# Kernel tuning notes

Measured on AMD Instinct MI355X. Metric: run time of the kernel, lower is better.

The kernel has to match this reference:

```python
import jax, jax.numpy as jnp
import numpy as np

D_MODEL = 1024
N_HEADS = 16
D_HEAD = D_MODEL // N_HEADS
SCALE = 1.0 / np.sqrt(D_HEAD).astype(np.float32)


def _feature_map(x):
    # phi(x) = elu(x) + 1
    return jax.nn.elu(x) + 1.0


def setup_inputs() -> dict:
    key = jax.random.key(0)
    ks = jax.random.split(key, 7)
    b, s = 4, 2048
    w = 1.0 / np.sqrt(D_MODEL).astype(np.float32)
    return {
        "x": jax.random.normal(ks[0], (b, s, D_MODEL), dtype=jnp.float32),
        "Wq": jax.random.normal(ks[1], (D_MODEL, D_MODEL), dtype=jnp.float32) * w,
        "Wk": jax.random.normal(ks[2], (D_MODEL, D_MODEL), dtype=jnp.float32) * w,
        "Wv": jax.random.normal(ks[3], (D_MODEL, D_MODEL), dtype=jnp.float32) * w,
        "Wo": jax.random.normal(ks[4], (D_MODEL, D_MODEL), dtype=jnp.float32) * w,
        "Wg": jax.random.normal(ks[5], (N_HEADS, D_MODEL), dtype=jnp.float32) * w,
        "bg": jax.random.normal(ks[6], (N_HEADS,), dtype=jnp.float32) * 0.02,
    }


def reference(x, Wq, Wk, Wv, Wo, Wg, bg):
    b, s, _ = x.shape
    # projections (PyTorch Linear: y = x @ W.T)
    q = (x @ Wq.T).reshape(b, s, N_HEADS, D_HEAD)
    k = (x @ Wk.T).reshape(b, s, N_HEADS, D_HEAD)
    v = (x @ Wv.T).reshape(b, s, N_HEADS, D_HEAD)
    q = _feature_map(q * SCALE)
    k = _feature_map(k)
    gate = jax.nn.sigmoid(x @ Wg.T + bg)  # [b, s, h]

    # time-major for scan: [s, b, h, dh] and [s, b, h]
    qt = jnp.moveaxis(q, 1, 0)
    kt = jnp.moveaxis(k, 1, 0)
    vt = jnp.moveaxis(v, 1, 0)
    gt = jnp.moveaxis(gate, 1, 0)

    S0 = jnp.zeros((b, N_HEADS, D_HEAD, D_HEAD), dtype=x.dtype)

    def step(S, inp):
        q_t, k_t, v_t, g_t = inp
        # S_t = g_t * S_{t-1} + k_t v_t^T
        S = g_t[:, :, None, None] * S + k_t[..., :, None] * v_t[..., None, :]
        y_t = jnp.einsum("bhi,bhij->bhj", q_t, S)
        return S, y_t

    _, ys = jax.lax.scan(step, S0, (qt, kt, vt, gt))  # ys: [s, b, h, dh]
    y = jnp.moveaxis(ys, 0, 1).reshape(b, s, D_MODEL)
    return y @ Wo.T
```

## Files before the change

### kernel.cpp

```cpp
#include <hip/hip_runtime.h>
#include <hip/hip_bf16.h>
#include <math.h>

#define BATCH 4
#define SEQ 2048
#define DMODEL 1024
#define NHEADS 16
#define DHEAD 64
#define MTOK (BATCH * SEQ)
#define SCALE_Q 0.125f
#define NCHAIN (BATCH * NHEADS)
#define CT 64
#define NC (SEQ / CT)
#define SP 72
#define QKVS 3072

typedef unsigned short ushort_t;
typedef __attribute__((ext_vector_type(8))) short bf16x8;
typedef __attribute__((ext_vector_type(4))) float f32x4;

__device__ __forceinline__ float bf2f(unsigned short u) {
    return __uint_as_float(((unsigned)u) << 16);
}
__device__ __forceinline__ unsigned short f2bf(float f) {
    unsigned u = __float_as_uint(f);
    return (unsigned short)((u + 0x7fffu + ((u >> 16) & 1u)) >> 16);
}

__global__ __launch_bounds__(256) void cvt_f32_bf16(const float* __restrict__ in,
                                                    ushort_t* __restrict__ out, int n4) {
    int i = blockIdx.x * 256 + threadIdx.x;
    if (i < n4) {
        float4 v = ((const float4*)in)[i];
        ushort4 o;
        o.x = f2bf(v.x); o.y = f2bf(v.y); o.z = f2bf(v.z); o.w = f2bf(v.w);
        ((ushort4*)out)[i] = o;
    }
}

__global__ __launch_bounds__(256) void cvt_weights(const float* __restrict__ Wq,
                                                   const float* __restrict__ Wk,
                                                   const float* __restrict__ Wv,
                                                   const float* __restrict__ Wo,
                                                   ushort_t* __restrict__ dst) {
    int i = blockIdx.x * 256 + threadIdx.x;
    const int row = i >> 8;
    const int c4 = i & 255;
    const float* src;
    if (row < 1024)      src = Wq + (size_t)row * DMODEL;
    else if (row < 2048) src = Wk + (size_t)(row - 1024) * DMODEL;
    else if (row < 3072) src = Wv + (size_t)(row - 2048) * DMODEL;
    else                 src = Wo + (size_t)(row - 3072) * DMODEL;
    float4 v = ((const float4*)src)[c4];
    ushort4 o;
    o.x = f2bf(v.x); o.y = f2bf(v.y); o.z = f2bf(v.z); o.w = f2bf(v.w);
    ((ushort4*)(dst + (size_t)row * DMODEL))[c4] = o;
}

#define GT 128
#define GBK 32

__global__ __launch_bounds__(256) void gemm_bf16(const ushort_t* __restrict__ A,
                                                 const ushort_t* __restrict__ B,
                                                 float* __restrict__ Cf,
                                                 ushort_t* __restrict__ Cb,
                                                 int M, int N, int K,
                                                 int mode) {
    __shared__ ushort_t As[GT * GBK];
    __shared__ ushort_t Bs[GT * GBK];

    const int tid = threadIdx.x;
    const int w = tid >> 6;
    const int l = tid & 63;
    const int m0 = blockIdx.y * GT;
    const int n0 = blockIdx.x * GT;
    const int wm = (w >> 1) * 64;
    const int wn = (w & 1) * 64;

    const int srow = l >> 2;
    const int schunk = (l & 3) * 8;

    f32x4 acc[4][4];
#pragma unroll
    for (int i = 0; i < 4; ++i)
#pragma unroll
        for (int j = 0; j < 4; ++j)
#pragma unroll
            for (int r = 0; r < 4; ++r) acc[i][j][r] = 0.f;

    const int fr = l & 15;
    const int fq = (l >> 4) * 8;

    for (int k0 = 0; k0 < K; k0 += GBK) {
        __syncthreads();
#pragma unroll
        for (int i = 0; i < 2; ++i) {
            const int s = w * 2 + i;
            const ushort_t* ga = A + (size_t)(m0 + s * 16 + srow) * K + k0 + schunk;
            const ushort_t* gb = B + (size_t)(n0 + s * 16 + srow) * K + k0 + schunk;
            __builtin_amdgcn_global_load_lds(
                (const __attribute__((address_space(1))) unsigned int*)(const void*)ga,
                (__attribute__((address_space(3))) unsigned int*)(void*)&As[s * 16 * GBK],
                16, 0, 0);
            __builtin_amdgcn_global_load_lds(
                (const __attribute__((address_space(1))) unsigned int*)(const void*)gb,
                (__attribute__((address_space(3))) unsigned int*)(void*)&Bs[s * 16 * GBK],
                16, 0, 0);
        }
        __syncthreads();

        bf16x8 af[4], bfr[4];
#pragma unroll
        for (int ti = 0; ti < 4; ++ti)
            af[ti] = *(const bf16x8*)&As[(wm + ti * 16 + fr) * GBK + fq];
#pragma unroll
        for (int tj = 0; tj < 4; ++tj)
            bfr[tj] = *(const bf16x8*)&Bs[(wn + tj * 16 + fr) * GBK + fq];
#pragma unroll
        for (int ti = 0; ti < 4; ++ti)
#pragma unroll
            for (int tj = 0; tj < 4; ++tj)
                acc[ti][tj] = __builtin_amdgcn_mfma_f32_16x16x32_bf16(
                    af[ti], bfr[tj], acc[ti][tj], 0, 0, 0);
    }

    float escale = 1.0f;
    bool do_phi = false;
    if (mode == 3) {
        do_phi = (n0 < 2048);
        escale = (n0 < 1024) ? SCALE_Q : 1.0f;
    }

    const int er = (l >> 4) * 4;
    const int ec = l & 15;
#pragma unroll
    for (int ti = 0; ti < 4; ++ti)
#pragma unroll
        for (int tj = 0; tj < 4; ++tj)
#pragma unroll
            for (int r = 0; r < 4; ++r) {
                const int row = m0 + wm + ti * 16 + er + r;
                const int col = n0 + wn + tj * 16 + ec;
                float val = acc[ti][tj][r];
                if (mode == 0) {
                    Cf[(size_t)row * N + col] = val;
                } else {
                    val *= escale;
                    if (do_phi) val = (val > 0.f) ? (val + 1.f) : __expf(val);
                    Cb[(size_t)row * N + col] = f2bf(val);
                }
            }
}

__global__ __launch_bounds__(256) void gate_kernel(const float* __restrict__ x,
                                                   const float* __restrict__ Wg,
                                                   const float* __restrict__ bg,
                                                   float* __restrict__ gate) {
    const int m = blockIdx.x;
    const int tid = threadIdx.x;
    const int h = tid >> 4;
    const int r = tid & 15;

    const float* xr = x + (size_t)m * DMODEL;
    const float* wr = Wg + (size_t)h * DMODEL;

    float p = 0.f;
#pragma unroll
    for (int i = 0; i < 16; ++i) {
        const int k = (r << 2) + (i << 6);
        float4 xv = *(const float4*)&xr[k];
        float4 wv = *(const float4*)&wr[k];
        p += xv.x * wv.x + xv.y * wv.y + xv.z * wv.z + xv.w * wv.w;
    }
    p += __shfl_xor(p, 8, 64);
    p += __shfl_xor(p, 4, 64);
    p += __shfl_xor(p, 2, 64);
    p += __shfl_xor(p, 1, 64);
    if (r == 0) {
        float vv = p + bg[h];
        gate[(size_t)m * NHEADS + h] = 1.f / (1.f + __expf(-vv));
    }
}

__global__ __launch_bounds__(256) void p1_kernel(const ushort_t* __restrict__ qkv,
                                                 const float* __restrict__ gate,
                                                 float* __restrict__ Dt,
                                                 float* __restrict__ Bg) {
    const int tile = blockIdx.x;
    const int chain = tile >> 5;
    const int c = tile & 31;
    const int b = chain >> 4;
    const int h = chain & 15;
    const int tid = threadIdx.x;
    const int w = tid >> 6;
    const int l = tid & 63;

    __shared__ ushort_t Ks[CT * SP];
    __shared__ ushort_t Vs[CT * SP];
    __shared__ float bs[CT];

    {
        const int row = tid >> 2;
        const int seg = (tid & 3) * 16;
        const size_t grow = ((size_t)(b * SEQ + c * CT + row)) * QKVS + h * DHEAD + seg;
        float4 a0 = *(const float4*)&qkv[grow + 1024];
        float4 a1 = *(const float4*)&qkv[grow + 1024 + 8];
        float4 b0 = *(const float4*)&qkv[grow + 2048];
        float4 b1 = *(const float4*)&qkv[grow + 2048 + 8];
        *(float4*)&Ks[row * SP + seg]     = a0;
        *(float4*)&Ks[row * SP + seg + 8] = a1;
        *(float4*)&Vs[row * SP + seg]     = b0;
        *(float4*)&Vs[row * SP + seg + 8] = b1;
    }
    if (tid < 64) {
        float g = gate[((size_t)(b * SEQ + c * CT + tid)) * NHEADS + h];
        float lg = __logf(g);
#pragma unroll
        for (int d = 1; d < 64; d <<= 1) {
            float n = __shfl_up(lg, d, 64);
            if (l >= d) lg += n;
        }
        bs[tid] = lg;
        if (tid == 63) Bg[tile] = lg;
    }
    __syncthreads();

    const float B = bs[63];
    const int fr = l & 15;
    const int fq = (l >> 4) * 8;
    const int jw = w * 16;

    f32x4 accD[4];
#pragma unroll
    for (int nt = 0; nt < 4; ++nt)
#pragma unroll
        for (int r = 0; r < 4; ++r) accD[nt][r] = 0.f;

#pragma unroll
    for (int kc = 0; kc < 2; ++kc) {
        float ef[8];
#pragma unroll
        for (int m = 0; m < 8; ++m) ef[m] = __expf(B - bs[kc * 32 + fq + m]);
        bf16x8 va;
#pragma unroll
        for (int m = 0; m < 8; ++m)
            va[m] = (short)Vs[(kc * 32 + fq + m) * SP + jw + fr];
#pragma unroll
        for (int nt = 0; nt < 4; ++nt) {
            bf16x8 kf;
#pragma unroll
            for (int m = 0; m < 8; ++m)
                kf[m] = (short)f2bf(ef[m] * bf2f(Ks[(kc * 32 + fq + m) * SP + nt * 16 + fr]));
            accD[nt] = __builtin_amdgcn_mfma_f32_16x16x32_bf16(va, kf, accD[nt], 0, 0, 0);
        }
    }

    const int er = (l >> 4) * 4;
    const size_t dbase = (size_t)tile * (DHEAD * DHEAD);
#pragma unroll
    for (int nt = 0; nt < 4; ++nt)
#pragma unroll
        for (int r = 0; r < 4; ++r) {
            const int j = jw + er + r;
            const int i = nt * 16 + fr;
            Dt[dbase + j * DHEAD + i] = accD[nt][r];
        }
}

__global__ __launch_bounds__(256) void p2_kernel(const float* __restrict__ Dt,
                                                 const float* __restrict__ Bg,
                                                 ushort_t* __restrict__ St) {
    const int chain = blockIdx.x >> 2;
    const int jq = (blockIdx.x & 3) * 16;
    const int tid = threadIdx.x;
    const int jj = jq + (tid >> 4);
    const int ii = (tid & 15) * 4;

    float4 S = make_float4(0.f, 0.f, 0.f, 0.f);
    for (int c = 0; c < NC; ++c) {
        const size_t base = (((size_t)chain * NC + c) * DHEAD + jj) * DHEAD + ii;
        ushort4 o;
        o.x = f2bf(S.x); o.y = f2bf(S.y); o.z = f2bf(S.z); o.w = f2bf(S.w);
        *(ushort4*)&St[base] = o;
        const float eB = __expf(Bg[chain * NC + c]);
        const float4 D = *(const float4*)&Dt[base];
        S.x = eB * S.x + D.x;
        S.y = eB * S.y + D.y;
        S.z = eB * S.z + D.z;
        S.w = eB * S.w + D.w;
    }
}

__global__ __launch_bounds__(256) void p3_kernel(const ushort_t* __restrict__ qkv,
                                                 const ushort_t* __restrict__ St,
                                                 const float* __restrict__ gate,
                                                 ushort_t* __restrict__ yb) {
    const int tile = blockIdx.x;
    const int chain = tile >> 5;
    const int c = tile & 31;
    const int b = chain >> 4;
    const int h = chain & 15;
    const int tid = threadIdx.x;
    const int w = tid >> 6;
    const int l = tid & 63;

    __shared__ ushort_t Qs[CT * SP];
    __shared__ ushort_t Ks[CT * SP];
    __shared__ ushort_t Vs[CT * SP];
    __shared__ ushort_t Ss[CT * SP];
    __shared__ ushort_t Ps[CT * SP];
    __shared__ float bs[CT];

    {
        const int row = tid >> 2;
        const int seg = (tid & 3) * 16;
        const size_t grow = ((size_t)(b * SEQ + c * CT + row)) * QKVS + h * DHEAD + seg;
        float4 q0 = *(const float4*)&qkv[grow];
        float4 q1 = *(const float4*)&qkv[grow + 8];
        float4 k0 = *(const float4*)&qkv[grow + 1024];
        float4 k1 = *(const float4*)&qkv[grow + 1024 + 8];
        float4 v0 = *(const float4*)&qkv[grow + 2048];
        float4 v1 = *(const float4*)&qkv[grow + 2048 + 8];
        const size_t srow = (((size_t)chain * NC + c) * DHEAD + row) * DHEAD + seg;
        float4 s0 = *(const float4*)&St[srow];
        float4 s1 = *(const float4*)&St[srow + 8];
        *(float4*)&Qs[row * SP + seg]     = q0;
        *(float4*)&Qs[row * SP + seg + 8] = q1;
        *(float4*)&Ks[row * SP + seg]     = k0;
        *(float4*)&Ks[row * SP + seg + 8] = k1;
        *(float4*)&Vs[row * SP + seg]     = v0;
        *(float4*)&Vs[row * SP + seg + 8] = v1;
        *(float4*)&Ss[row * SP + seg]     = s0;
        *(float4*)&Ss[row * SP + seg + 8] = s1;
    }
    if (tid < 64) {
        float g = gate[((size_t)(b * SEQ + c * CT + tid)) * NHEADS + h];
        float lg = __logf(g);
#pragma unroll
        for (int d = 1; d < 64; d <<= 1) {
            float n = __shfl_up(lg, d, 64);
            if (l >= d) lg += n;
        }
        bs[tid] = lg;
    }
    __syncthreads();

    const int fr = l & 15;
    const int fq = (l >> 4) * 8;
    const int tw = w * 16;

    bf16x8 qa[2];
#pragma unroll
    for (int kc = 0; kc < 2; ++kc)
        qa[kc] = *(const bf16x8*)&Qs[(tw + fr) * SP + kc * 32 + fq];

    f32x4 accA[4], accP[4];
#pragma unroll
    for (int nt = 0; nt < 4; ++nt)
#pragma unroll
        for (int r = 0; r < 4; ++r) { accA[nt][r] = 0.f; accP[nt][r] = 0.f; }

#pragma unroll
    for (int kc = 0; kc < 2; ++kc)
#pragma unroll
        for (int nt = 0; nt < 4; ++nt) {
            bf16x8 sb = *(const bf16x8*)&Ss[(nt * 16 + fr) * SP + kc * 32 + fq];
            accA[nt] = __builtin_amdgcn_mfma_f32_16x16x32_bf16(qa[kc], sb, accA[nt], 0, 0, 0);
            bf16x8 kf = *(const bf16x8*)&Ks[(nt * 16 + fr) * SP + kc * 32 + fq];
            accP[nt] = __builtin_amdgcn_mfma_f32_16x16x32_bf16(qa[kc], kf, accP[nt], 0, 0, 0);
        }

    const int er = (l >> 4) * 4;
    int trow[4];
    float bt[4];
#pragma unroll
    for (int r = 0; r < 4; ++r) { trow[r] = tw + er + r; bt[r] = bs[trow[r]]; }
#pragma unroll
    for (int nt = 0; nt < 4; ++nt) {
        const int tau = nt * 16 + fr;
        const float btau = bs[tau];
#pragma unroll
        for (int r = 0; r < 4; ++r) {
            float f = (tau <= trow[r]) ? __expf(bt[r] - btau) : 0.f;
            Ps[trow[r] * SP + tau] = f2bf(accP[nt][r] * f);
        }
    }
    __syncthreads();

    f32x4 accY[4];
#pragma unroll
    for (int r = 0; r < 4; ++r) {
        const float eb = __expf(bt[r]);
#pragma unroll
        for (int nt = 0; nt < 4; ++nt) accY[nt][r] = accA[nt][r] * eb;
    }
#pragma unroll
    for (int kc = 0; kc < 2; ++kc) {
        bf16x8 pa = *(const bf16x8*)&Ps[(tw + fr) * SP + kc * 32 + fq];
#pragma unroll
        for (int nt = 0; nt < 4; ++nt) {
            bf16x8 vf;
#pragma unroll
            for (int m = 0; m < 8; ++m)
                vf[m] = (short)Vs[(kc * 32 + fq + m) * SP + nt * 16 + fr];
            accY[nt] = __builtin_amdgcn_mfma_f32_16x16x32_bf16(pa, vf, accY[nt], 0, 0, 0);
        }
    }

    const size_t ybase = ((size_t)(b * SEQ + c * CT)) * DMODEL + h * DHEAD;
#pragma unroll
    for (int nt = 0; nt < 4; ++nt)
#pragma unroll
        for (int r = 0; r < 4; ++r)
            yb[ybase + (size_t)trow[r] * DMODEL + nt * 16 + fr] = f2bf(accY[nt][r]);
}

extern "C" void kernel_launch(void* const* d_in, const int* in_sizes, int n_in,
                              void* d_out, int out_size, void* d_ws, size_t ws_size,
                              hipStream_t stream) {
    const float* x  = (const float*)d_in[0];
    const float* Wq = (const float*)d_in[1];
    const float* Wk = (const float*)d_in[2];
    const float* Wv = (const float*)d_in[3];
    const float* Wo = (const float*)d_in[4];
    const float* Wg = (const float*)d_in[5];
    const float* bg = (const float*)d_in[6];
    float* out = (float*)d_out;

    const size_t elems = (size_t)MTOK * DMODEL;
    const size_t welems = (size_t)DMODEL * DMODEL;
    const size_t stelems = (size_t)NCHAIN * NC * DHEAD * DHEAD;

    ushort_t* xb   = (ushort_t*)d_ws;
    ushort_t* qkv  = xb + elems;
    ushort_t* yb   = qkv + (size_t)MTOK * QKVS;
    ushort_t* wcat = yb + elems;
    float* gate    = (float*)(wcat + 4 * welems);
    ushort_t* St   = (ushort_t*)(gate + (size_t)MTOK * NHEADS);
    float* Bg      = (float*)(St + stelems);
    float* Dt      = Bg + (size_t)NCHAIN * NC;

    const size_t need = (size_t)((char*)(Dt + stelems) - (char*)d_ws);
    if (ws_size < need) return;

    cvt_f32_bf16<<<dim3((int)(elems / 4 / 256)), dim3(256), 0, stream>>>(x, xb, (int)(elems / 4));
    cvt_weights<<<dim3((int)(4 * welems / 4 / 256)), dim3(256), 0, stream>>>(Wq, Wk, Wv, Wo, wcat);

    gemm_bf16<<<dim3(QKVS / GT, MTOK / GT), dim3(256), 0, stream>>>(
        xb, wcat, nullptr, qkv, MTOK, QKVS, DMODEL, 3);

    gate_kernel<<<dim3(MTOK), dim3(256), 0, stream>>>(x, Wg, bg, gate);

    p1_kernel<<<dim3(NCHAIN * NC), dim3(256), 0, stream>>>(qkv, gate, Dt, Bg);
    p2_kernel<<<dim3(NCHAIN * 4), dim3(256), 0, stream>>>(Dt, Bg, St);
    p3_kernel<<<dim3(NCHAIN * NC), dim3(256), 0, stream>>>(qkv, St, gate, yb);

    gemm_bf16<<<dim3(DMODEL / GT, MTOK / GT), dim3(256), 0, stream>>>(
        yb, wcat + 3 * welems, out, nullptr, MTOK, DMODEL, DMODEL, 0);
}
```

Baseline: 286.6 us.

## Double-buffer GEMM LDS tiles and XOR-swizzle shared-memory layout

The bf16 MFMA GEMM now keeps two LDS stages and issues the global-to-LDS loads for the next K tile before computing on the current one. This cuts the loop to one barrier per iteration and lets memory traffic overlap the MFMAs. It also XOR-swizzles the 16-byte chunk positions within each LDS row, on both the write and read sides, to reduce bank conflicts on fragment loads. The workspace is compacted by aliasing St onto the x buffer and yb onto Dt. This doubles LDS use per block and relies on the compiler's waitcnt handling for the async LDS loads to stay correct.

```diff
diff --git a/kernel.cpp b/kernel.cpp
--- a/kernel.cpp
+++ b/kernel.cpp
@@ -66,8 +66,8 @@
                                                  ushort_t* __restrict__ Cb,
                                                  int M, int N, int K,
                                                  int mode) {
-    __shared__ ushort_t As[GT * GBK];
-    __shared__ ushort_t Bs[GT * GBK];
+    __shared__ ushort_t As[2][GT * GBK];
+    __shared__ ushort_t Bs[2][GT * GBK];
 
     const int tid = threadIdx.x;
     const int w = tid >> 6;
@@ -78,7 +78,32 @@
     const int wn = (w & 1) * 64;
 
     const int srow = l >> 2;
-    const int schunk = (l & 3) * 8;
+    const int schunk = ((l & 3) ^ ((l >> 3) & 3)) * 8;
+
+    const ushort_t* aseg[2];
+    const ushort_t* bseg[2];
+#pragma unroll
+    for (int i = 0; i < 2; ++i) {
+        const int s = w * 2 + i;
+        aseg[i] = A + (size_t)(m0 + s * 16 + srow) * K + schunk;
+        bseg[i] = B + (size_t)(n0 + s * 16 + srow) * K + schunk;
+    }
+
+#define STAGE(buf, k0)                                                          \
+    do {                                                                        \
+        _Pragma("unroll")                                                       \
+        for (int i_ = 0; i_ < 2; ++i_) {                                        \
+            const int s_ = w * 2 + i_;                                          \
+            __builtin_amdgcn_global_load_lds(                                   \
+                (const __attribute__((address_space(1))) unsigned int*)(const void*)(aseg[i_] + (k0)), \
+                (__attribute__((address_space(3))) unsigned int*)(void*)&As[buf][s_ * 16 * GBK], \
+                16, 0, 0);                                                      \
+            __builtin_amdgcn_global_load_lds(                                   \
+                (const __attribute__((address_space(1))) unsigned int*)(const void*)(bseg[i_] + (k0)), \
+                (__attribute__((address_space(3))) unsigned int*)(void*)&Bs[buf][s_ * 16 * GBK], \
+                16, 0, 0);                                                      \
+        }                                                                       \
+    } while (0)
 
     f32x4 acc[4][4];
 #pragma unroll
@@ -89,33 +114,25 @@
             for (int r = 0; r < 4; ++r) acc[i][j][r] = 0.f;
 
     const int fr = l & 15;
-    const int fq = (l >> 4) * 8;
-
-    for (int k0 = 0; k0 < K; k0 += GBK) {
+    const int fsw = (((l >> 4) ^ ((fr >> 1) & 3))) * 8;
+
+    STAGE(0, 0);
+
+    const int nit = K / GBK;
+    for (int it = 0; it < nit; ++it) {
         __syncthreads();
-#pragma unroll
-        for (int i = 0; i < 2; ++i) {
-            const int s = w * 2 + i;
-            const ushort_t* ga = A + (size_t)(m0 + s * 16 + srow) * K + k0 + schunk;
-            const ushort_t* gb = B + (size_t)(n0 + s * 16 + srow) * K + k0 + schunk;
-            __builtin_amdgcn_global_load_lds(
-                (const __attribute__((address_space(1))) unsigned int*)(const void*)ga,
-                (__attribute__((address_space(3))) unsigned int*)(void*)&As[s * 16 * GBK],
-                16, 0, 0);
-            __builtin_amdgcn_global_load_lds(
-                (const __attribute__((address_space(1))) unsigned int*)(const void*)gb,
-                (__attribute__((address_space(3))) unsigned int*)(void*)&Bs[s * 16 * GBK],
-                16, 0, 0);
-        }
-        __syncthreads();
+        if (it + 1 < nit) STAGE((it + 1) & 1, (it + 1) * GBK);
+
+        const ushort_t* __restrict__ as = As[it & 1];
+        const ushort_t* __restrict__ bs = Bs[it & 1];
 
         bf16x8 af[4], bfr[4];
 #pragma unroll
         for (int ti = 0; ti < 4; ++ti)
-            af[ti] = *(const bf16x8*)&As[(wm + ti * 16 + fr) * GBK + fq];
+            af[ti] = *(const bf16x8*)&as[(wm + ti * 16 + fr) * GBK + fsw];
 #pragma unroll
         for (int tj = 0; tj < 4; ++tj)
-            bfr[tj] = *(const bf16x8*)&Bs[(wn + tj * 16 + fr) * GBK + fq];
+            bfr[tj] = *(const bf16x8*)&bs[(wn + tj * 16 + fr) * GBK + fsw];
 #pragma unroll
         for (int ti = 0; ti < 4; ++ti)
 #pragma unroll
@@ -123,6 +140,7 @@
                 acc[ti][tj] = __builtin_amdgcn_mfma_f32_16x16x32_bf16(
                     af[ti], bfr[tj], acc[ti][tj], 0, 0, 0);
     }
+#undef STAGE
 
     float escale = 1.0f;
     bool do_phi = false;
@@ -432,13 +450,13 @@
     const size_t stelems = (size_t)NCHAIN * NC * DHEAD * DHEAD;
 
     ushort_t* xb   = (ushort_t*)d_ws;
+    ushort_t* St   = xb;
     ushort_t* qkv  = xb + elems;
-    ushort_t* yb   = qkv + (size_t)MTOK * QKVS;
-    ushort_t* wcat = yb + elems;
+    ushort_t* wcat = qkv + (size_t)MTOK * QKVS;
     float* gate    = (float*)(wcat + 4 * welems);
-    ushort_t* St   = (ushort_t*)(gate + (size_t)MTOK * NHEADS);
-    float* Bg      = (float*)(St + stelems);
+    float* Bg      = gate + (size_t)MTOK * NHEADS;
     float* Dt      = Bg + (size_t)NCHAIN * NC;
+    ushort_t* yb   = (ushort_t*)Dt;
 
     const size_t need = (size_t)((char*)(Dt + stelems) - (char*)d_ws);
     if (ws_size < need) return;
```

After: 268.2 us. -6.4%, faster.
